# Performance work log

Hardware: AMD Instinct MI355X
Metric: run time of the kernel (lower is better)

The kernel has to match this reference:

```python
import jax, jax.numpy as jnp
import numpy as np

WS = 8        # window size
NH = 8        # num heads


def setup_inputs() -> dict:
    key = jax.random.key(0)
    ks = jax.random.split(key, 6)
    B, C, H, W = 8, 256, 64, 64
    Cr = C // 4
    s = lambda n: 1.0 / np.sqrt(n)
    return {
        "x": jax.random.normal(ks[0], (B, C, H, W), jnp.float32),
        "ca_w1": jax.random.normal(ks[1], (Cr, C), jnp.float32) * s(C),
        "ca_b1": jnp.zeros((Cr,), jnp.float32),
        "ca_w2": jax.random.normal(ks[2], (C, Cr), jnp.float32) * s(Cr),
        "ca_b2": jnp.zeros((C,), jnp.float32),
        "in_proj_w": jax.random.normal(ks[3], (3 * C, C), jnp.float32) * s(C),
        "in_proj_b": jnp.zeros((3 * C,), jnp.float32),
        "out_proj_w": jax.random.normal(ks[4], (C, C), jnp.float32) * s(C),
        "out_proj_b": jnp.zeros((C,), jnp.float32),
    }


def reference(x, ca_w1, ca_b1, ca_w2, ca_b2, in_proj_w, in_proj_b, out_proj_w, out_proj_b):
    B, C, H, W = x.shape
    # ---- channel SE gate: AdaptiveAvgPool2d(1) -> 1x1 conv == linear ----
    pooled = x.mean(axis=(2, 3))                                   # [B, C]
    h1 = jax.nn.relu(pooled @ ca_w1.T + ca_b1)                     # [B, C/4]
    ca = jax.nn.sigmoid(h1 @ ca_w2.T + ca_b2)                      # [B, C]
    x = x * ca[:, :, None, None]

    # ---- window partition (non-overlapping unfold) ----
    Hw, Ww = H // WS, W // WS
    nwin = Hw * Ww
    xw = x.reshape(B, C, Hw, WS, Ww, WS).transpose(0, 1, 2, 4, 3, 5)   # [B,C,Hw,Ww,ws,ws]
    # view(B,C,nwin,ws*ws).permute(2,0,3,1).reshape(nwin*B, ws*ws, C)
    xw = xw.reshape(B, C, nwin, WS * WS).transpose(2, 0, 3, 1).reshape(nwin * B, WS * WS, C)

    # ---- nn.MultiheadAttention with batch_first=False: (L, N, E) ----
    # L = nwin*B (sequence!), N = ws*ws (batch!), E = C  -- faithful to source quirk
    L, N, _ = xw.shape
    hd = C // NH
    qkv = xw @ in_proj_w.T + in_proj_b                             # [L, N, 3C]
    q, k, v = jnp.split(qkv, 3, axis=-1)
    to_heads = lambda t: t.reshape(L, N, NH, hd).transpose(1, 2, 0, 3)  # [N, NH, L, hd]
    q, k, v = to_heads(q), to_heads(k), to_heads(v)
    scale = 1.0 / jnp.sqrt(jnp.asarray(hd, x.dtype))
    attn = jax.nn.softmax(jnp.einsum("nhld,nhmd->nhlm", q * scale, k), axis=-1)
    o = jnp.einsum("nhlm,nhmd->nhld", attn, v)                     # [N, NH, L, hd]
    o = o.transpose(2, 0, 1, 3).reshape(L, N, C)
    o = o @ out_proj_w.T + out_proj_b                              # [L, N, C]

    # ---- reshape back; nearest interpolate H*W -> H*W is identity ----
    o = o.reshape(nwin, B, WS * WS, C).transpose(1, 3, 0, 2)       # [B, C, nwin, ws*ws]
    x_out = o.reshape(B, C, H, W)
    return x + x_out
```

## Files before the change

kernel.cpp:

```cpp
#include <hip/hip_runtime.h>
#include <hip/hip_bf16.h>
#include <math.h>


typedef unsigned short ushort_t;
typedef unsigned int uint_t;
typedef __attribute__((ext_vector_type(8))) short bf16x8;
typedef __attribute__((ext_vector_type(4))) float f32x4;

#define ALPHA 0.25503486f

__device__ __forceinline__ uint_t pk_rne(float a, float b) {
    __hip_bfloat16 ha = __float2bfloat16(a), hb = __float2bfloat16(b);
    ushort_t ua = *(ushort_t*)&ha, ub = *(ushort_t*)&hb;
    return (uint_t)ua | ((uint_t)ub << 16);
}

__device__ __forceinline__ uint_t pk2(float a, float b) {
    union { float f; uint_t u; } ua, ub; ua.f = a; ub.f = b;
    return __builtin_amdgcn_perm(ua.u, ub.u, 0x03020706u);
}

__device__ __forceinline__ float bfh(uint_t h) {
    union { uint_t u; float f; } t; t.u = h << 16; return t.f;
}

__device__ __forceinline__ void gl_lds16(const ushort_t* g, ushort_t* l) {
    __builtin_amdgcn_global_load_lds(
        (__attribute__((address_space(1))) unsigned int*)(g),
        (__attribute__((address_space(3))) unsigned int*)(l), 16, 0, 0);
}

__global__ __launch_bounds__(256) void k_pre(const float* __restrict__ x,
                                             float* __restrict__ pooled,
                                             const float* __restrict__ ipw,
                                             ushort_t* __restrict__ Wqb,
                                             const float* __restrict__ opw,
                                             ushort_t* __restrict__ Wob) {
    int bx = blockIdx.x;
    int t = threadIdx.x;
    if (bx < 2048) {
        const float4* row4 = (const float4*)(x + (size_t)bx * 4096);
        float s = 0.f;
        for (int i = t; i < 1024; i += 256) {
            float4 v = row4[i];
            s += v.x + v.y + v.z + v.w;
        }
        __shared__ float red[256];
        red[t] = s;
        __syncthreads();
        for (int o = 128; o > 0; o >>= 1) {
            if (t < o) red[t] += red[t + o];
            __syncthreads();
        }
        if (t == 0) pooled[bx] = red[0] * (1.f / 4096.f);
    } else if (bx < 2144) {
        int i = (bx - 2048) * 256 + t;
        float sc = (i < 8192) ? ALPHA : 1.f;
        const float4* s4 = (const float4*)ipw + (size_t)i * 2;
        float4 a = s4[0], b = s4[1];
        uint4 u;
        u.x = pk_rne(a.x * sc, a.y * sc); u.y = pk_rne(a.z * sc, a.w * sc);
        u.z = pk_rne(b.x * sc, b.y * sc); u.w = pk_rne(b.z * sc, b.w * sc);
        *(uint4*)(Wqb + (size_t)i * 8) = u;
    } else {
        int i = (bx - 2144) * 256 + t;
        const float4* s4 = (const float4*)opw + (size_t)i * 2;
        float4 a = s4[0], b = s4[1];
        uint4 u;
        u.x = pk_rne(a.x, a.y); u.y = pk_rne(a.z, a.w);
        u.z = pk_rne(b.x, b.y); u.w = pk_rne(b.z, b.w);
        *(uint4*)(Wob + (size_t)i * 8) = u;
    }
}

__global__ __launch_bounds__(256) void k_cvt(const float* __restrict__ src,
                                             ushort_t* __restrict__ dst, int n8,
                                             int scale_n8, float scale) {
    int i = blockIdx.x * 256 + threadIdx.x;
    if (i >= n8) return;
    float sc = (i < scale_n8) ? scale : 1.f;
    const float4* s = (const float4*)src + (size_t)i * 2;
    float4 a = s[0], b = s[1];
    uint4 u;
    u.x = pk_rne(a.x * sc, a.y * sc); u.y = pk_rne(a.z * sc, a.w * sc);
    u.z = pk_rne(b.x * sc, b.y * sc); u.w = pk_rne(b.z * sc, b.w * sc);
    *(uint4*)(dst + (size_t)i * 8) = u;
}

__global__ __launch_bounds__(256) void k_se(const float* __restrict__ pooled,
                                            const float* __restrict__ w1,
                                            const float* __restrict__ b1,
                                            const float* __restrict__ w2,
                                            const float* __restrict__ b2,
                                            float* __restrict__ ca) {
    __shared__ float sp[2048];
    __shared__ float sh1[512];
    int t = threadIdx.x;
    for (int i = t; i < 2048; i += 256) sp[i] = pooled[i];
    __syncthreads();
    for (int o = t; o < 512; o += 256) {
        int b = o >> 6, m = o & 63;
        float s = b1[m];
        const float* wr = w1 + (size_t)m * 256;
        const float* pr = sp + b * 256;
        for (int c = 0; c < 256; c++) s += pr[c] * wr[c];
        sh1[o] = s > 0.f ? s : 0.f;
    }
    __syncthreads();
    for (int o = t; o < 2048; o += 256) {
        int b = o >> 8, m = o & 255;
        float s = b2[m];
        const float* wr = w2 + (size_t)m * 64;
        const float* hr = sh1 + b * 64;
        for (int c = 0; c < 64; c++) s += hr[c] * wr[c];
        ca[o] = 1.f / (1.f + __expf(-s));
    }
}

#define GPAD 524
__global__ __launch_bounds__(256) void k_gate(const float* __restrict__ x,
                                              const float* __restrict__ pooled,
                                              const float* __restrict__ w1,
                                              const float* __restrict__ b1,
                                              const float* __restrict__ w2,
                                              const float* __restrict__ b2,
                                              ushort_t* __restrict__ Ab) {
    __shared__ __align__(16) ushort_t Ls[32 * GPAD];
    __shared__ float sh1[64];
    __shared__ float sca[32];
    int bx = blockIdx.x;
    int b = bx >> 6, hw = (bx >> 3) & 7, c0 = (bx & 7) * 32;
    int t = threadIdx.x;
    if (t < 64) {
        float s = b1[t];
        const float4* wr = (const float4*)(w1 + (size_t)t * 256);
        const float4* pr = (const float4*)(pooled + b * 256);
        for (int c = 0; c < 64; c++) {
            float4 wv = wr[c], pv = pr[c];
            s += pv.x * wv.x + pv.y * wv.y + pv.z * wv.z + pv.w * wv.w;
        }
        sh1[t] = s > 0.f ? s : 0.f;
    }
    __syncthreads();
    if (t < 32) {
        int m = c0 + t;
        float s = b2[m];
        const float* wr = w2 + (size_t)m * 64;
        for (int j = 0; j < 64; j++) s += sh1[j] * wr[j];
        sca[t] = 1.f / (1.f + __expf(-s));
    }
    __syncthreads();
    const float4* xb = (const float4*)(x + ((size_t)(b * 256 + c0) * 64 + hw * 8) * 64);
#pragma unroll
    for (int i = 0; i < 16; i++) {
        int f = i * 256 + t;
        int ch = f >> 7, rem = f & 127, r = rem >> 4, w4 = rem & 15;
        float4 v = xb[(size_t)ch * 1024 + r * 16 + w4];
        float g = sca[ch];
        uint2 u;
        u.x = pk_rne(v.x * g, v.y * g);
        u.y = pk_rne(v.z * g, v.w * g);
        *(uint2*)&Ls[ch * GPAD + r * 64 + w4 * 4] = u;
    }
    __syncthreads();
#pragma unroll
    for (int i = 0; i < 8; i++) {
        int q = i * 256 + t;
        int rr = q >> 2, part = q & 3;
        int ww = rr >> 6, p = rr & 63;
        int px = (p >> 3) * 64 + ww * 8 + (p & 7);
        const ushort_t* ls = &Ls[part * 8 * GPAD + px];
        uint4 u;
        u.x = (uint_t)ls[0]        | ((uint_t)ls[GPAD] << 16);
        u.y = (uint_t)ls[2 * GPAD] | ((uint_t)ls[3 * GPAD] << 16);
        u.z = (uint_t)ls[4 * GPAD] | ((uint_t)ls[5 * GPAD] << 16);
        u.w = (uint_t)ls[6 * GPAD] | ((uint_t)ls[7 * GPAD] << 16);
        size_t m = (size_t)(((hw * 8 + ww) * 8 + b) * 64 + p);
        *(uint4*)(Ab + m * 256 + c0 + part * 8) = u;
    }
}

__global__ __launch_bounds__(256, 3) void k_gemm_qkv4(const ushort_t* __restrict__ A,
                                                      const ushort_t* __restrict__ Bw,
                                                      const float* __restrict__ bias,
                                                      ushort_t* __restrict__ Qb,
                                                      ushort_t* __restrict__ Kb,
                                                      ushort_t* __restrict__ Vb) {
    __shared__ __align__(16) ushort_t As[2][4096];
    __shared__ __align__(16) ushort_t Bs[2][8192];
    int tid = threadIdx.x;
    int lane = tid & 63, wave = tid >> 6;
    int wm = wave >> 1, wn = wave & 1;
    int col = lane & 15, quad = lane >> 4;
    int orig = blockIdx.x;
    int xcd = orig & 7;
    int i384 = orig >> 3;
    int mi = i384 / 6;
    int r6 = i384 - mi * 6;
    int sec = r6 >> 1, nh = r6 & 1;
    int m0 = (xcd * 64 + mi) * 64;
    const ushort_t* Bsec = Bw + ((size_t)sec << 16) + ((size_t)nh * 128) * 256;

    int cbase = wave * 64 + lane;
    const ushort_t* asrc[2];
    const ushort_t* bsrc[4];
#pragma unroll
    for (int q = 0; q < 2; q++) {
        int c = q * 256 + cbase;
        int row = c >> 3;
        int kp = (c & 7) ^ (row & 7);
        asrc[q] = A + (size_t)(m0 + row) * 256 + kp * 8;
    }
#pragma unroll
    for (int q = 0; q < 4; q++) {
        int c = q * 256 + cbase;
        int row = c >> 3;
        int kp = (c & 7) ^ (row & 7);
        bsrc[q] = Bsec + (size_t)row * 256 + kp * 8;
    }

    f32x4 acc[2][4];
#pragma unroll
    for (int i = 0; i < 2; i++)
#pragma unroll
        for (int j = 0; j < 4; j++) acc[i][j] = (f32x4){0.f, 0.f, 0.f, 0.f};

    for (int t2 = 0; t2 < 2; t2++) {
        int k0 = t2 * 128;
#pragma unroll
        for (int h = 0; h < 2; h++) {
#pragma unroll
            for (int q = 0; q < 2; q++)
                gl_lds16(asrc[q] + k0 + h * 64, &As[h][(q * 4 + wave) * 512]);
#pragma unroll
            for (int q = 0; q < 4; q++)
                gl_lds16(bsrc[q] + k0 + h * 64, &Bs[h][(q * 4 + wave) * 512]);
        }
        __syncthreads();
#pragma unroll
        for (int h = 0; h < 2; h++) {
            const ushort_t* Ac = As[h];
            const ushort_t* Bc = Bs[h];
#pragma unroll
            for (int kk = 0; kk < 2; kk++) {
                bf16x8 af[2], bfg[4];
#pragma unroll
                for (int i = 0; i < 2; i++) {
                    int row = wm * 32 + i * 16 + col;
                    af[i] = *(const bf16x8*)&Ac[row * 64 + ((kk * 4 + quad) ^ (row & 7)) * 8];
                }
#pragma unroll
                for (int j = 0; j < 4; j++) {
                    int row = wn * 64 + j * 16 + col;
                    bfg[j] = *(const bf16x8*)&Bc[row * 64 + ((kk * 4 + quad) ^ (row & 7)) * 8];
                }
#pragma unroll
                for (int i = 0; i < 2; i++)
#pragma unroll
                    for (int j = 0; j < 4; j++)
                        acc[i][j] = __builtin_amdgcn_mfma_f32_16x16x32_bf16(bfg[j], af[i], acc[i][j], 0, 0, 0);
            }
        }
        __syncthreads();
    }

    ushort_t* dst = (sec == 0) ? Qb : (sec == 1) ? Kb : Vb;
    float bsc = (sec == 0) ? ALPHA : 1.f;
    int nb0 = nh * 128 + wn * 64 + quad * 4;
#pragma unroll
    for (int j = 0; j < 4; j++) {
        float4 bv = *(const float4*)(bias + sec * 256 + nb0 + j * 16);
        bv.x *= bsc; bv.y *= bsc; bv.z *= bsc; bv.w *= bsc;
#pragma unroll
        for (int i = 0; i < 2; i++) {
            int m = m0 + wm * 32 + i * 16 + col;
            uint2 st;
            st.x = pk_rne(acc[i][j][0] + bv.x, acc[i][j][1] + bv.y);
            st.y = pk_rne(acc[i][j][2] + bv.z, acc[i][j][3] + bv.w);
            *(uint2*)(dst + (size_t)m * 256 + nb0 + j * 16) = st;
        }
    }
}

__global__ __launch_bounds__(512, 4) void k_attn(const ushort_t* __restrict__ Qb,
                                                 const ushort_t* __restrict__ Kb,
                                                 const ushort_t* __restrict__ Vb,
                                                 ushort_t* __restrict__ AO) {
    __shared__ __align__(16) ushort_t Ks[512 * 32];
    __shared__ __align__(16) ushort_t Vt[32 * 512];
    int p = blockIdx.x >> 3, h = blockIdx.x & 7;
    int tid = threadIdx.x;
    int lane = tid & 63, wave = tid >> 6;
    int col = lane & 15, quad = lane >> 4;

#pragma unroll
    for (int it = 0; it < 4; it++) {
        int u = it * 512 + tid;
        int key = u >> 2, oct = u & 3;
        size_t grow = ((size_t)(key * 64 + p)) * 256 + h * 32 + oct * 8;
        int ck = oct ^ ((key >> 3) & 3);
        *(bf16x8*)&Ks[key * 32 + ck * 8] = *(const bf16x8*)(Kb + grow);
    }
#pragma unroll
    for (int it = 0; it < 2; it++) {
        int u = it * 512 + tid;
        int kp = u >> 2, oct = u & 3;
        int k0 = kp * 2;
        size_t g0 = ((size_t)(k0 * 64 + p)) * 256 + h * 32 + oct * 8;
        bf16x8 v0 = *(const bf16x8*)(Vb + g0);
        bf16x8 v1 = *(const bf16x8*)(Vb + g0 + 16384);
        int kc = kp >> 2;
#pragma unroll
        for (int j = 0; j < 8; j++) {
            int vc = oct * 8 + j;
            int kcs = kc ^ (vc & 7) ^ ((vc >> 3) << 1);
            uint_t pkv = (uint_t)(ushort_t)v0[j] | ((uint_t)(ushort_t)v1[j] << 16);
            *(uint_t*)&Vt[vc * 512 + kcs * 8 + (k0 & 7)] = pkv;
        }
    }

    bf16x8 qfrag[4];
#pragma unroll
    for (int i = 0; i < 4; i++) {
        int qt = wave * 4 + i;
        qfrag[i] = *(const bf16x8*)(Qb + ((size_t)((qt * 16 + col) * 64 + p)) * 256 + h * 32 + quad * 8);
    }

    f32x4 O0[4], O1[4], accS[4];
#pragma unroll
    for (int i = 0; i < 4; i++) {
        O0[i] = (f32x4){0.f, 0.f, 0.f, 0.f};
        O1[i] = (f32x4){0.f, 0.f, 0.f, 0.f};
        accS[i] = (f32x4){0.f, 0.f, 0.f, 0.f};
    }
    const f32x4 zero = {0.f, 0.f, 0.f, 0.f};
    const short OB = (short)0x3F80;
    const bf16x8 ones8 = {OB, OB, OB, OB, OB, OB, OB, OB};
    int R = col >> 2, r4 = lane & 3;
    int krow0 = 8 * R + r4;
    int vc0 = col, vc1 = col + 16;
    int sw0 = (vc0 & 7) ^ ((vc0 >> 3) << 1);
    int sw1 = (vc1 & 7) ^ ((vc1 >> 3) << 1);

    __syncthreads();

    for (int c = 0; c < 512; c += 32) {
        int row0 = c + krow0;
        int row1 = row0 + 4;
        int ckq = quad ^ ((row0 >> 3) & 3);
        bf16x8 kf0 = *(const bf16x8*)&Ks[row0 * 32 + ckq * 8];
        bf16x8 kf1 = *(const bf16x8*)&Ks[row1 * 32 + ckq * 8];
        int kc = (c >> 3) + quad;
        bf16x8 vf0 = *(const bf16x8*)&Vt[vc0 * 512 + ((kc ^ sw0) * 8)];
        bf16x8 vf1 = *(const bf16x8*)&Vt[vc1 * 512 + ((kc ^ sw1) * 8)];
#pragma unroll
        for (int i = 0; i < 4; i++) {
            __builtin_amdgcn_s_setprio(1);
            f32x4 s0 = __builtin_amdgcn_mfma_f32_16x16x32_bf16(kf0, qfrag[i], zero, 0, 0, 0);
            f32x4 s1 = __builtin_amdgcn_mfma_f32_16x16x32_bf16(kf1, qfrag[i], zero, 0, 0, 0);
            __builtin_amdgcn_s_setprio(0);
            float p0[4], p1[4];
#pragma unroll
            for (int r = 0; r < 4; r++) {
                p0[r] = __builtin_amdgcn_exp2f(s0[r]);
                p1[r] = __builtin_amdgcn_exp2f(s1[r]);
            }
            union { uint_t u[4]; bf16x8 v; } pb;
            pb.u[0] = pk2(p0[0], p0[1]);
            pb.u[1] = pk2(p0[2], p0[3]);
            pb.u[2] = pk2(p1[0], p1[1]);
            pb.u[3] = pk2(p1[2], p1[3]);
            __builtin_amdgcn_s_setprio(1);
            O0[i] = __builtin_amdgcn_mfma_f32_16x16x32_bf16(vf0, pb.v, O0[i], 0, 0, 0);
            O1[i] = __builtin_amdgcn_mfma_f32_16x16x32_bf16(vf1, pb.v, O1[i], 0, 0, 0);
            accS[i] = __builtin_amdgcn_mfma_f32_16x16x32_bf16(ones8, pb.v, accS[i], 0, 0, 0);
            __builtin_amdgcn_s_setprio(0);
        }
    }

#pragma unroll
    for (int i = 0; i < 4; i++) {
        float inv = 1.f / accS[i][0];
        int qt = wave * 4 + i;
        ushort_t* dst = AO + ((size_t)((qt * 16 + col) * 64 + p)) * 256 + h * 32;
        uint2 st0, st1;
        st0.x = pk_rne(O0[i][0] * inv, O0[i][1] * inv);
        st0.y = pk_rne(O0[i][2] * inv, O0[i][3] * inv);
        st1.x = pk_rne(O1[i][0] * inv, O1[i][1] * inv);
        st1.y = pk_rne(O1[i][2] * inv, O1[i][3] * inv);
        *(uint2*)(dst + quad * 4) = st0;
        *(uint2*)(dst + 16 + quad * 4) = st1;
    }
}

__global__ __launch_bounds__(256, 4) void k_gemm_out3(const ushort_t* __restrict__ A,
                                                      const ushort_t* __restrict__ Bw,
                                                      const float* __restrict__ bias,
                                                      const ushort_t* __restrict__ G,
                                                      const float* __restrict__ x,
                                                      const float* __restrict__ ca,
                                                      float* __restrict__ out) {
    __shared__ __align__(16) ushort_t As[4096];
    __shared__ __align__(16) ushort_t Bs[8192];
    int tid = threadIdx.x;
    int lane = tid & 63, wave = tid >> 6;
    int wm = wave >> 1, wn = wave & 1;
    int col = lane & 15, quad = lane >> 4;
    int orig = blockIdx.x;
    int xcd = orig & 7;
    int i128 = orig >> 3;
    int mi = i128 >> 1;
    int ns = i128 & 1;
    int m0 = (xcd * 64 + mi) * 64;
    int n0 = ns * 128;

    int cbase = wave * 64 + lane;
    const ushort_t* asrc[2];
    const ushort_t* bsrc[4];
#pragma unroll
    for (int q = 0; q < 2; q++) {
        int c = q * 256 + cbase;
        int row = c >> 3;
        int kp = (c & 7) ^ (row & 7);
        asrc[q] = A + (size_t)(m0 + row) * 256 + kp * 8;
    }
#pragma unroll
    for (int q = 0; q < 4; q++) {
        int c = q * 256 + cbase;
        int row = c >> 3;
        int kp = (c & 7) ^ (row & 7);
        bsrc[q] = Bw + (size_t)(n0 + row) * 256 + kp * 8;
    }

    f32x4 acc[2][4];
#pragma unroll
    for (int i = 0; i < 2; i++)
#pragma unroll
        for (int j = 0; j < 4; j++) acc[i][j] = (f32x4){0.f, 0.f, 0.f, 0.f};

    for (int t = 0; t < 4; t++) {
        int k0 = t * 64;
#pragma unroll
        for (int q = 0; q < 2; q++) gl_lds16(asrc[q] + k0, &As[(q * 4 + wave) * 512]);
#pragma unroll
        for (int q = 0; q < 4; q++) gl_lds16(bsrc[q] + k0, &Bs[(q * 4 + wave) * 512]);
        __syncthreads();
#pragma unroll
        for (int kk = 0; kk < 2; kk++) {
            bf16x8 af[2], bfg[4];
#pragma unroll
            for (int i = 0; i < 2; i++) {
                int row = wm * 32 + i * 16 + col;
                af[i] = *(const bf16x8*)&As[row * 64 + ((kk * 4 + quad) ^ (row & 7)) * 8];
            }
#pragma unroll
            for (int j = 0; j < 4; j++) {
                int row = wn * 64 + j * 16 + col;
                bfg[j] = *(const bf16x8*)&Bs[row * 64 + ((kk * 4 + quad) ^ (row & 7)) * 8];
            }
#pragma unroll
            for (int i = 0; i < 2; i++)
#pragma unroll
                for (int j = 0; j < 4; j++)
                    acc[i][j] = __builtin_amdgcn_mfma_f32_16x16x32_bf16(bfg[j], af[i], acc[i][j], 0, 0, 0);
        }
        __syncthreads();
    }

    int lw = m0 >> 6;
    int b = lw & 7, w_idx = lw >> 3;
    int hw = w_idx >> 3, ww = w_idx & 7;
    if (G != nullptr) {
#pragma unroll
        for (int j = 0; j < 4; j++) {
            int nbase = n0 + wn * 64 + j * 16 + quad * 4;
            float4 bv = *(const float4*)(bias + nbase);
#pragma unroll
            for (int i = 0; i < 2; i++) {
                int px = wm * 32 + i * 16 + col;
                int mres = ((hw * 8 + (px >> 3)) * 8 + b) * 64 + ww * 8 + (px & 7);
                uint2 gv = *(const uint2*)(G + (size_t)mres * 256 + nbase);
                float g0 = bfh(gv.x & 0xffffu), g1 = bfh(gv.x >> 16);
                float g2 = bfh(gv.y & 0xffffu), g3 = bfh(gv.y >> 16);
                size_t ob = (((size_t)b * 256 + nbase) * 64 + w_idx) * 64 + px;
                out[ob]            = acc[i][j][0] + bv.x + g0;
                out[ob + 4096]     = acc[i][j][1] + bv.y + g1;
                out[ob + 2 * 4096] = acc[i][j][2] + bv.z + g2;
                out[ob + 3 * 4096] = acc[i][j][3] + bv.w + g3;
            }
        }
    } else {
#pragma unroll
        for (int j = 0; j < 4; j++) {
            int nbase = n0 + wn * 64 + j * 16 + quad * 4;
            float4 bv = *(const float4*)(bias + nbase);
            float4 cv = *(const float4*)(ca + b * 256 + nbase);
#pragma unroll
            for (int i = 0; i < 2; i++) {
                int px = wm * 32 + i * 16 + col;
#pragma unroll
                for (int r = 0; r < 4; r++) {
                    int n = nbase + r;
                    float bias_r = (r == 0) ? bv.x : (r == 1) ? bv.y : (r == 2) ? bv.z : bv.w;
                    float ca_r = (r == 0) ? cv.x : (r == 1) ? cv.y : (r == 2) ? cv.z : cv.w;
                    size_t oi = (((size_t)b * 256 + n) * 64 + w_idx) * 64 + px;
                    out[oi] = acc[i][j][r] + bias_r + x[oi] * ca_r;
                }
            }
        }
    }
}

extern "C" void kernel_launch(void* const* d_in, const int* in_sizes, int n_in,
                              void* d_out, int out_size, void* d_ws, size_t ws_size,
                              hipStream_t stream) {
    const float* x     = (const float*)d_in[0];
    const float* ca_w1 = (const float*)d_in[1];
    const float* ca_b1 = (const float*)d_in[2];
    const float* ca_w2 = (const float*)d_in[3];
    const float* ca_b2 = (const float*)d_in[4];
    const float* ipw   = (const float*)d_in[5];
    const float* ipb   = (const float*)d_in[6];
    const float* opw   = (const float*)d_in[7];
    const float* opb   = (const float*)d_in[8];
    float* out = (float*)d_out;

    char* ws = (char*)d_ws;
    const size_t MB16 = 16777216ull;
    ushort_t* Qb = (ushort_t*)(ws + 0);
    ushort_t* Kb = (ushort_t*)(ws + MB16);
    ushort_t* Vb = (ushort_t*)(ws + 2 * MB16);
    float* pooled = (float*)(ws + 3 * MB16);
    float* ca     = (float*)(ws + 3 * MB16 + 8192);

    const size_t WOB_OFF = 3 * MB16 + 16384;
    const size_t WQB_OFF = 3 * MB16 + 163840;
    const size_t AB_OFF  = 3 * MB16 + 1048576;
    bool big_ws = (ws_size >= AB_OFF + MB16);

    ushort_t* Wob, *Wqb, *Ab;
    const ushort_t* G;
    if (big_ws) {
        Wob = (ushort_t*)(ws + WOB_OFF);
        Wqb = (ushort_t*)(ws + WQB_OFF);
        Ab  = (ushort_t*)(ws + AB_OFF);
        G   = Ab;
    } else {
        Ab  = (ushort_t*)d_out;
        Wqb = (ushort_t*)((char*)d_out + MB16);
        Wob = Vb;
        G   = nullptr;
    }

    k_pre<<<big_ws ? 2176 : 2144, 256, 0, stream>>>(x, pooled, ipw, Wqb, opw, Wob);
    if (!big_ws) k_se<<<1, 256, 0, stream>>>(pooled, ca_w1, ca_b1, ca_w2, ca_b2, ca);
    k_gate<<<512, 256, 0, stream>>>(x, pooled, ca_w1, ca_b1, ca_w2, ca_b2, Ab);
    k_gemm_qkv4<<<3072, 256, 0, stream>>>(Ab, Wqb, ipb, Qb, Kb, Vb);
    k_attn<<<512, 512, 0, stream>>>(Qb, Kb, Vb, Qb );
    if (!big_ws) k_cvt<<<32, 256, 0, stream>>>(opw, Vb, 8192, 0, 1.f);
    k_gemm_out3<<<1024, 256, 0, stream>>>(Qb, Wob, opb, G, x, ca, out);
}
```

Before: 183.2 us.

## Fold SE channel gate into per-batch QKV weights and fuse pooling into permute

The separate pooling pass over x is removed. Per-channel partial sums are now computed inside the permute kernel, which writes the ungated bf16 activations. A new kernel finishes the SE MLP and folds the sigmoid gate into a per-batch copy of the in-projection weights, so the QKV GEMM selects weights by batch. The residual in the output GEMM now multiplies by the gate explicitly. This saves one full read of x, at the cost of an 8x larger weight buffer and per-batch weight traffic in the GEMM.

```diff
diff --git a/kernel.cpp b/kernel.cpp
--- a/kernel.cpp
+++ b/kernel.cpp
@@ -29,49 +29,6 @@
     __builtin_amdgcn_global_load_lds(
         (__attribute__((address_space(1))) unsigned int*)(g),
         (__attribute__((address_space(3))) unsigned int*)(l), 16, 0, 0);
-}
-
-__global__ __launch_bounds__(256) void k_pre(const float* __restrict__ x,
-                                             float* __restrict__ pooled,
-                                             const float* __restrict__ ipw,
-                                             ushort_t* __restrict__ Wqb,
-                                             const float* __restrict__ opw,
-                                             ushort_t* __restrict__ Wob) {
-    int bx = blockIdx.x;
-    int t = threadIdx.x;
-    if (bx < 2048) {
-        const float4* row4 = (const float4*)(x + (size_t)bx * 4096);
-        float s = 0.f;
-        for (int i = t; i < 1024; i += 256) {
-            float4 v = row4[i];
-            s += v.x + v.y + v.z + v.w;
-        }
-        __shared__ float red[256];
-        red[t] = s;
-        __syncthreads();
-        for (int o = 128; o > 0; o >>= 1) {
-            if (t < o) red[t] += red[t + o];
-            __syncthreads();
-        }
-        if (t == 0) pooled[bx] = red[0] * (1.f / 4096.f);
-    } else if (bx < 2144) {
-        int i = (bx - 2048) * 256 + t;
-        float sc = (i < 8192) ? ALPHA : 1.f;
-        const float4* s4 = (const float4*)ipw + (size_t)i * 2;
-        float4 a = s4[0], b = s4[1];
-        uint4 u;
-        u.x = pk_rne(a.x * sc, a.y * sc); u.y = pk_rne(a.z * sc, a.w * sc);
-        u.z = pk_rne(b.x * sc, b.y * sc); u.w = pk_rne(b.z * sc, b.w * sc);
-        *(uint4*)(Wqb + (size_t)i * 8) = u;
-    } else {
-        int i = (bx - 2144) * 256 + t;
-        const float4* s4 = (const float4*)opw + (size_t)i * 2;
-        float4 a = s4[0], b = s4[1];
-        uint4 u;
-        u.x = pk_rne(a.x, a.y); u.y = pk_rne(a.z, a.w);
-        u.z = pk_rne(b.x, b.y); u.w = pk_rne(b.z, b.w);
-        *(uint4*)(Wob + (size_t)i * 8) = u;
-    }
 }
 
 __global__ __launch_bounds__(256) void k_cvt(const float* __restrict__ src,
@@ -88,81 +45,35 @@
     *(uint4*)(dst + (size_t)i * 8) = u;
 }
 
-__global__ __launch_bounds__(256) void k_se(const float* __restrict__ pooled,
-                                            const float* __restrict__ w1,
-                                            const float* __restrict__ b1,
-                                            const float* __restrict__ w2,
-                                            const float* __restrict__ b2,
-                                            float* __restrict__ ca) {
-    __shared__ float sp[2048];
-    __shared__ float sh1[512];
-    int t = threadIdx.x;
-    for (int i = t; i < 2048; i += 256) sp[i] = pooled[i];
-    __syncthreads();
-    for (int o = t; o < 512; o += 256) {
-        int b = o >> 6, m = o & 63;
-        float s = b1[m];
-        const float* wr = w1 + (size_t)m * 256;
-        const float* pr = sp + b * 256;
-        for (int c = 0; c < 256; c++) s += pr[c] * wr[c];
-        sh1[o] = s > 0.f ? s : 0.f;
-    }
-    __syncthreads();
-    for (int o = t; o < 2048; o += 256) {
-        int b = o >> 8, m = o & 255;
-        float s = b2[m];
-        const float* wr = w2 + (size_t)m * 64;
-        const float* hr = sh1 + b * 64;
-        for (int c = 0; c < 64; c++) s += hr[c] * wr[c];
-        ca[o] = 1.f / (1.f + __expf(-s));
-    }
-}
-
 #define GPAD 524
-__global__ __launch_bounds__(256) void k_gate(const float* __restrict__ x,
-                                              const float* __restrict__ pooled,
-                                              const float* __restrict__ w1,
-                                              const float* __restrict__ b1,
-                                              const float* __restrict__ w2,
-                                              const float* __restrict__ b2,
-                                              ushort_t* __restrict__ Ab) {
+__global__ __launch_bounds__(256) void k_perm(const float* __restrict__ x,
+                                              ushort_t* __restrict__ Abu,
+                                              float* __restrict__ partials) {
     __shared__ __align__(16) ushort_t Ls[32 * GPAD];
-    __shared__ float sh1[64];
-    __shared__ float sca[32];
+    __shared__ float sred[256];
     int bx = blockIdx.x;
     int b = bx >> 6, hw = (bx >> 3) & 7, c0 = (bx & 7) * 32;
     int t = threadIdx.x;
-    if (t < 64) {
-        float s = b1[t];
-        const float4* wr = (const float4*)(w1 + (size_t)t * 256);
-        const float4* pr = (const float4*)(pooled + b * 256);
-        for (int c = 0; c < 64; c++) {
-            float4 wv = wr[c], pv = pr[c];
-            s += pv.x * wv.x + pv.y * wv.y + pv.z * wv.z + pv.w * wv.w;
-        }
-        sh1[t] = s > 0.f ? s : 0.f;
-    }
+    int ch = t >> 3, s = t & 7;
+    const float4* xc = (const float4*)(x + ((size_t)(b * 256 + c0 + ch) * 64 + hw * 8) * 64);
+    float psum = 0.f;
+#pragma unroll
+    for (int j = 0; j < 16; j++) {
+        int u = j * 8 + s;
+        float4 v = xc[u];
+        psum += (v.x + v.y) + (v.z + v.w);
+        uint2 uu;
+        uu.x = pk_rne(v.x, v.y);
+        uu.y = pk_rne(v.z, v.w);
+        *(uint2*)&Ls[ch * GPAD + u * 4] = uu;
+    }
+    sred[t] = psum;
     __syncthreads();
-    if (t < 32) {
-        int m = c0 + t;
-        float s = b2[m];
-        const float* wr = w2 + (size_t)m * 64;
-        for (int j = 0; j < 64; j++) s += sh1[j] * wr[j];
-        sca[t] = 1.f / (1.f + __expf(-s));
-    }
+    if (s < 4) sred[t] += sred[t + 4];
     __syncthreads();
-    const float4* xb = (const float4*)(x + ((size_t)(b * 256 + c0) * 64 + hw * 8) * 64);
-#pragma unroll
-    for (int i = 0; i < 16; i++) {
-        int f = i * 256 + t;
-        int ch = f >> 7, rem = f & 127, r = rem >> 4, w4 = rem & 15;
-        float4 v = xb[(size_t)ch * 1024 + r * 16 + w4];
-        float g = sca[ch];
-        uint2 u;
-        u.x = pk_rne(v.x * g, v.y * g);
-        u.y = pk_rne(v.z * g, v.w * g);
-        *(uint2*)&Ls[ch * GPAD + r * 64 + w4 * 4] = u;
-    }
+    if (s < 2) sred[t] += sred[t + 2];
+    __syncthreads();
+    if (s == 0) partials[((size_t)(b * 256 + c0 + ch)) * 8 + hw] = sred[t] + sred[t + 1];
     __syncthreads();
 #pragma unroll
     for (int i = 0; i < 8; i++) {
@@ -177,7 +88,67 @@
         u.z = (uint_t)ls[4 * GPAD] | ((uint_t)ls[5 * GPAD] << 16);
         u.w = (uint_t)ls[6 * GPAD] | ((uint_t)ls[7 * GPAD] << 16);
         size_t m = (size_t)(((hw * 8 + ww) * 8 + b) * 64 + p);
-        *(uint4*)(Ab + m * 256 + c0 + part * 8) = u;
+        *(uint4*)(Abu + m * 256 + c0 + part * 8) = u;
+    }
+}
+
+__global__ __launch_bounds__(256) void k_wcvt(const float* __restrict__ ipw,
+                                              const float* __restrict__ w1,
+                                              const float* __restrict__ b1,
+                                              const float* __restrict__ w2,
+                                              const float* __restrict__ b2,
+                                              const float* __restrict__ partials,
+                                              ushort_t* __restrict__ Wqb8,
+                                              float* __restrict__ ca_out,
+                                              const float* __restrict__ opw,
+                                              ushort_t* __restrict__ Wob) {
+    int bx = blockIdx.x;
+    int t = threadIdx.x;
+    if (bx < 768) {
+        __shared__ float sp[256];
+        __shared__ float sh1[64];
+        __shared__ float sca[256];
+        int b = bx / 96, lb = bx - b * 96;
+        {
+            const float* pp = partials + ((size_t)(b * 256 + t)) * 8;
+            float s = ((pp[0] + pp[1]) + (pp[2] + pp[3])) + ((pp[4] + pp[5]) + (pp[6] + pp[7]));
+            sp[t] = s * (1.f / 4096.f);
+        }
+        __syncthreads();
+        if (t < 64) {
+            float s = b1[t];
+            const float* wr = w1 + (size_t)t * 256;
+            for (int c = 0; c < 256; c++) s += sp[c] * wr[c];
+            sh1[t] = s > 0.f ? s : 0.f;
+        }
+        __syncthreads();
+        {
+            float s = b2[t];
+            const float* wr = w2 + (size_t)t * 64;
+            for (int j = 0; j < 64; j++) s += sh1[j] * wr[j];
+            sca[t] = 1.f / (1.f + __expf(-s));
+        }
+        __syncthreads();
+        if (lb == 0) ca_out[b * 256 + t] = sca[t];
+        int i = lb * 256 + t;
+        int n = i >> 5, c0g = (i & 31) * 8;
+        float asec = (n < 256) ? ALPHA : 1.f;
+        const float4* s4 = (const float4*)(ipw + (size_t)n * 256 + c0g);
+        float4 a = s4[0], bb = s4[1];
+        uint4 u;
+        u.x = pk_rne(a.x * sca[c0g] * asec,      a.y * sca[c0g + 1] * asec);
+        u.y = pk_rne(a.z * sca[c0g + 2] * asec,  a.w * sca[c0g + 3] * asec);
+        u.z = pk_rne(bb.x * sca[c0g + 4] * asec, bb.y * sca[c0g + 5] * asec);
+        u.w = pk_rne(bb.z * sca[c0g + 6] * asec, bb.w * sca[c0g + 7] * asec);
+        *(uint4*)(Wqb8 + ((size_t)b * 24576 + i) * 8) = u;
+    } else {
+        int i = (bx - 768) * 256 + t;
+        const float4* s4 = (const float4*)opw + (size_t)i * 2;
+        float4 a = s4[0], b = s4[1];
+        uint4 u;
+        u.x = pk_rne(a.x, a.y); u.y = pk_rne(a.z, a.w);
+        u.z = pk_rne(b.x, b.y); u.w = pk_rne(b.z, b.w);
+        *(uint4*)(Wob + (size_t)i * 8) = u;
     }
 }
 
@@ -200,7 +171,8 @@
     int r6 = i384 - mi * 6;
     int sec = r6 >> 1, nh = r6 & 1;
     int m0 = (xcd * 64 + mi) * 64;
-    const ushort_t* Bsec = Bw + ((size_t)sec << 16) + ((size_t)nh * 128) * 256;
+    int b = mi & 7;
+    const ushort_t* Bsec = Bw + (size_t)b * 196608 + ((size_t)sec << 16) + ((size_t)nh * 128) * 256;
 
     int cbase = wave * 64 + lane;
     const ushort_t* asrc[2];
@@ -476,6 +448,7 @@
         for (int j = 0; j < 4; j++) {
             int nbase = n0 + wn * 64 + j * 16 + quad * 4;
             float4 bv = *(const float4*)(bias + nbase);
+            float4 cv = *(const float4*)(ca + b * 256 + nbase);
 #pragma unroll
             for (int i = 0; i < 2; i++) {
                 int px = wm * 32 + i * 16 + col;
@@ -484,10 +457,10 @@
                 float g0 = bfh(gv.x & 0xffffu), g1 = bfh(gv.x >> 16);
                 float g2 = bfh(gv.y & 0xffffu), g3 = bfh(gv.y >> 16);
                 size_t ob = (((size_t)b * 256 + nbase) * 64 + w_idx) * 64 + px;
-                out[ob]            = acc[i][j][0] + bv.x + g0;
-                out[ob + 4096]     = acc[i][j][1] + bv.y + g1;
-                out[ob + 2 * 4096] = acc[i][j][2] + bv.z + g2;
-                out[ob + 3 * 4096] = acc[i][j][3] + bv.w + g3;
+                out[ob]            = acc[i][j][0] + bv.x + g0 * cv.x;
+                out[ob + 4096]     = acc[i][j][1] + bv.y + g1 * cv.y;
+                out[ob + 2 * 4096] = acc[i][j][2] + bv.z + g2 * cv.z;
+                out[ob + 3 * 4096] = acc[i][j][3] + bv.w + g3 * cv.w;
             }
         }
     } else {
@@ -531,32 +504,32 @@
     ushort_t* Qb = (ushort_t*)(ws + 0);
     ushort_t* Kb = (ushort_t*)(ws + MB16);
     ushort_t* Vb = (ushort_t*)(ws + 2 * MB16);
-    float* pooled = (float*)(ws + 3 * MB16);
-    float* ca     = (float*)(ws + 3 * MB16 + 8192);
-
-    const size_t WOB_OFF = 3 * MB16 + 16384;
-    const size_t WQB_OFF = 3 * MB16 + 163840;
-    const size_t AB_OFF  = 3 * MB16 + 1048576;
-    bool big_ws = (ws_size >= AB_OFF + MB16);
-
-    ushort_t* Wob, *Wqb, *Ab;
+    const size_t SM = 3 * MB16;
+    float* ca       = (float*)(ws + SM);
+    float* partials = (float*)(ws + SM + 8192);
+    ushort_t* WobW  = (ushort_t*)(ws + SM + 131072);
+    const size_t WQB8_OFF = SM + 1048576;
+    const size_t ABU_OFF  = SM + 8 * 1048576;
+    bool big_ws = (ws_size >= ABU_OFF + MB16);
+
+    ushort_t *Wqb8, *Abu, *Wob;
     const ushort_t* G;
     if (big_ws) {
-        Wob = (ushort_t*)(ws + WOB_OFF);
-        Wqb = (ushort_t*)(ws + WQB_OFF);
-        Ab  = (ushort_t*)(ws + AB_OFF);
-        G   = Ab;
+        Wqb8 = (ushort_t*)(ws + WQB8_OFF);
+        Abu  = (ushort_t*)(ws + ABU_OFF);
+        Wob  = WobW;
+        G    = Abu;
     } else {
-        Ab  = (ushort_t*)d_out;
-        Wqb = (ushort_t*)((char*)d_out + MB16);
-        Wob = Vb;
-        G   = nullptr;
-    }
-
-    k_pre<<<big_ws ? 2176 : 2144, 256, 0, stream>>>(x, pooled, ipw, Wqb, opw, Wob);
-    if (!big_ws) k_se<<<1, 256, 0, stream>>>(pooled, ca_w1, ca_b1, ca_w2, ca_b2, ca);
-    k_gate<<<512, 256, 0, stream>>>(x, pooled, ca_w1, ca_b1, ca_w2, ca_b2, Ab);
-    k_gemm_qkv4<<<3072, 256, 0, stream>>>(Ab, Wqb, ipb, Qb, Kb, Vb);
+        Abu  = (ushort_t*)d_out;
+        Wqb8 = (ushort_t*)((char*)d_out + MB16);
+        Wob  = Vb;
+        G    = nullptr;
+    }
+
+    k_perm<<<512, 256, 0, stream>>>(x, Abu, partials);
+    k_wcvt<<<big_ws ? 800 : 768, 256, 0, stream>>>(ipw, ca_w1, ca_b1, ca_w2, ca_b2,
+                                                   partials, Wqb8, ca, opw, WobW);
+    k_gemm_qkv4<<<3072, 256, 0, stream>>>(Abu, Wqb8, ipb, Qb, Kb, Vb);
     k_attn<<<512, 512, 0, stream>>>(Qb, Kb, Vb, Qb );
     if (!big_ws) k_cvt<<<32, 256, 0, stream>>>(opw, Vb, 8192, 0, 1.f);
     k_gemm_out3<<<1024, 256, 0, stream>>>(Qb, Wob, opb, G, x, ca, out);
```

Result: slower. 188.9 us (+3.1%).
